# Kernel tuning notes

Hardware: AMD Instinct MI355X
Metric: run time of the kernel (lower is better)

## Reference

```python
import jax, jax.numpy as jnp
import numpy as np

EPS = 1e-5
QMAX = 127.0   # 8-bit symmetric: representable range [-128, 127]
QMIN = -128.0


def ste_round(x):
    # straight-through rounding (identity gradient)
    return x + jax.lax.stop_gradient(jnp.round(x) - x)


def setup_inputs() -> dict:
    key = jax.random.key(0)
    ks = jax.random.split(key, 7)
    N, C_in, C_out, H, W = 64, 256, 128, 56, 56
    x = jax.random.normal(ks[0], (N, C_in, H, W), jnp.float32)
    act_scaling_factor = jax.random.uniform(ks[1], (1,), jnp.float32, 0.02, 0.08)
    bn_weight = 1.0 + 0.3 * jax.random.normal(ks[2], (C_in,), jnp.float32)
    bn_bias = 0.1 * jax.random.normal(ks[3], (C_in,), jnp.float32)
    bn_mean = 0.1 * jax.random.normal(ks[4], (C_in,), jnp.float32)
    bn_var = jax.random.uniform(ks[5], (C_in,), jnp.float32, 0.5, 1.5)
    conv_weight = 0.05 * jax.random.normal(ks[6], (C_out, C_in, 1, 1), jnp.float32)
    return {
        "x": x,
        "act_scaling_factor": act_scaling_factor,
        "bn_weight": bn_weight,
        "bn_bias": bn_bias,
        "bn_mean": bn_mean,
        "bn_var": bn_var,
        "conv_weight": conv_weight,
    }


def _fwd(x, act_scaling_factor, bn_weight, bn_bias, bn_mean, bn_var, conv_weight):
    act_sf = act_scaling_factor.reshape(())

    # ---- QuantBn: fold BN, quantize folded scale per-channel (8-bit symmetric) ----
    inv_std = jax.lax.rsqrt(bn_var + EPS)
    scale = bn_weight * inv_std                    # [C_in]
    shift = bn_bias - bn_mean * scale              # [C_in]
    bn_sf = jnp.max(jnp.abs(scale)) / QMAX         # per-tensor bn weight scale
    scale_q = jnp.clip(ste_round(scale / bn_sf), QMIN, QMAX) * bn_sf
    bias_sf = bn_sf * act_sf                        # bias quantized at combined scale
    shift_q = ste_round(shift / bias_sf) * bias_sf
    x = x * scale_q[None, :, None, None] + shift_q[None, :, None, None]

    # ---- ReLU ----
    x = jnp.maximum(x, 0.0)

    # ---- QuantAct 1: per-tensor symmetric 8-bit requant ----
    sf1 = jnp.max(jnp.abs(x)) / QMAX
    x = jnp.clip(ste_round(x / sf1), QMIN, QMAX) * sf1

    # ---- QuantConv2d: per-output-channel 8-bit symmetric weight quant, 1x1 conv ----
    w_sf = jnp.max(jnp.abs(conv_weight), axis=(1, 2, 3)) / QMAX   # [C_out]
    w_q = jnp.clip(ste_round(conv_weight / w_sf[:, None, None, None]), QMIN, QMAX) \
          * w_sf[:, None, None, None]
    y = jax.lax.conv_general_dilated(
        x, w_q, window_strides=(1, 1), padding='VALID',
        dimension_numbers=('NCHW', 'OIHW', 'NCHW'))

    # ---- QuantAct 2 ----
    sf2 = jnp.max(jnp.abs(y)) / QMAX
    y = jnp.clip(ste_round(y / sf2), QMIN, QMAX) * sf2

    # ---- QuantAveragePool2d (2x2, stride 2): average in integer domain, re-round ----
    N, C, H, W = y.shape
    y_int = (y / sf2).reshape(N, C, H // 2, 2, W // 2, 2).mean(axis=(3, 5))
    out = ste_round(y_int) * sf2
    return out, sf2


def reference(x, act_scaling_factor, bn_weight, bn_bias, bn_mean, bn_var, conv_weight):
    return _fwd(x, act_scaling_factor, bn_weight, bn_bias, bn_mean, bn_var, conv_weight)
```

## Files before the change

### kernel.cpp

```cpp
#include <hip/hip_runtime.h>

#define QMAXF 127.0f
typedef int i32x4 __attribute__((ext_vector_type(4)));

__device__ __forceinline__ unsigned fkey(float f) {
  const unsigned b = __float_as_uint(f);
  return (b & 0x80000000u) ? ~b : (b | 0x80000000u);
}
__device__ __forceinline__ float fdec(unsigned u) {
  return __uint_as_float((u & 0x80000000u) ? (u & 0x7FFFFFFFu) : ~u);
}

__global__ __launch_bounds__(256, 8) void k1_minmax(
    const float* __restrict__ x, const float* __restrict__ actsf,
    const float* __restrict__ bnw, const float* __restrict__ bnb,
    const float* __restrict__ bnm, const float* __restrict__ bnv,
    const float* __restrict__ cw, unsigned* __restrict__ chanKmx,
    unsigned* __restrict__ chanKmn, float* __restrict__ scq,
    float* __restrict__ shq, float* __restrict__ wsf,
    signed char* __restrict__ wq8) {
  const int t = threadIdx.x, b = blockIdx.x;
  if (b == 2048) {
    __shared__ float red[4];
    float scale, shift;
    {
#pragma clang fp contract(off)
      float inv = 1.0f / sqrtf(bnv[t] + 1e-5f);
      scale = bnw[t] * inv;
      float tmp = bnm[t] * scale;
      shift = bnb[t] - tmp;
    }
    float a = fabsf(scale);
    for (int o = 32; o > 0; o >>= 1) a = fmaxf(a, __shfl_xor(a, o));
    if ((t & 63) == 0) red[t >> 6] = a;
    __syncthreads();
    const float amax = fmaxf(fmaxf(red[0], red[1]), fmaxf(red[2], red[3]));
    const float bn_sf = amax / QMAXF;
    scq[t] = fminf(fmaxf(rintf(scale / bn_sf), -128.f), 127.f) * bn_sf;
    const float bias_sf = bn_sf * actsf[0];
    shq[t] = rintf(shift / bias_sf) * bias_sf;
    const int r = t >> 1, half = t & 1;
    const float4* wrow = (const float4*)(cw + r * 256 + half * 128);
    float mx = 0.f;
#pragma unroll
    for (int j = 0; j < 32; ++j) {
      const float4 v = wrow[j];
      mx = fmaxf(mx, fmaxf(fmaxf(fabsf(v.x), fabsf(v.y)), fmaxf(fabsf(v.z), fabsf(v.w))));
    }
    mx = fmaxf(mx, __shfl_xor(mx, 1));
    const float wsf_v = mx / QMAXF;
    if (half == 0) wsf[r] = wsf_v;
    int* w8w = (int*)wq8;
#pragma unroll
    for (int j = 0; j < 32; ++j) {
      const float4 v = wrow[j];
      const float q0 = fminf(fmaxf(rintf(v.x / wsf_v), -128.f), 127.f);
      const float q1 = fminf(fmaxf(rintf(v.y / wsf_v), -128.f), 127.f);
      const float q2 = fminf(fmaxf(rintf(v.z / wsf_v), -128.f), 127.f);
      const float q3 = fminf(fmaxf(rintf(v.w / wsf_v), -128.f), 127.f);
      w8w[r * 64 + half * 32 + j] =
          ((int)q0 & 255) | (((int)q1 & 255) << 8) | (((int)q2 & 255) << 16) | (((int)q3 & 255) << 24);
    }
    return;
  }
  __shared__ float redmn[4][8], redmx[4][8];
  const int n = b >> 5, cg = b & 31;
  const float4* __restrict__ x4 = (const float4*)x + (long)(n * 256 + cg * 8) * 784;
  float mn[8], mx[8];
#pragma unroll
  for (int r = 0; r < 8; ++r) { mn[r] = __builtin_inff(); mx[r] = -__builtin_inff(); }
#pragma unroll
  for (int r = 0; r < 8; ++r) {
    const float4* row = x4 + r * 784;
    for (int j = t; j < 784; j += 256) {
      const float4 v = row[j];
      mn[r] = fminf(mn[r], fminf(fminf(v.x, v.y), fminf(v.z, v.w)));
      mx[r] = fmaxf(mx[r], fmaxf(fmaxf(v.x, v.y), fmaxf(v.z, v.w)));
    }
  }
#pragma unroll
  for (int r = 0; r < 8; ++r)
    for (int o = 32; o > 0; o >>= 1) {
      mn[r] = fminf(mn[r], __shfl_xor(mn[r], o));
      mx[r] = fmaxf(mx[r], __shfl_xor(mx[r], o));
    }
  if ((t & 63) == 0) {
#pragma unroll
    for (int r = 0; r < 8; ++r) { redmn[t >> 6][r] = mn[r]; redmx[t >> 6][r] = mx[r]; }
  }
  __syncthreads();
  if (t < 8) {
    const float fmn = fminf(fminf(redmn[0][t], redmn[1][t]), fminf(redmn[2][t], redmn[3][t]));
    const float fmx = fmaxf(fmaxf(redmx[0][t], redmx[1][t]), fmaxf(redmx[2][t], redmx[3][t]));
    atomicMax(&chanKmx[cg * 8 + t], fkey(fmx));
    atomicMax(&chanKmn[cg * 8 + t], ~fkey(fmn));
  }
}

__global__ __launch_bounds__(256, 4) void k2f_quant_gemm(
    const float* __restrict__ x, const float* __restrict__ scq,
    const float* __restrict__ shq, const unsigned* __restrict__ chanKmx,
    const unsigned* __restrict__ chanKmn, const signed char* __restrict__ wq8,
    const float* __restrict__ wsf, signed char* __restrict__ xqT,
    unsigned* __restrict__ gmax2K) {
  __shared__ int sw[64 * 64];
  __shared__ float comax[128];
  __shared__ float red[4];
  __shared__ float sf1s;
  const int t = threadIdx.x, w = t >> 6, l = t & 63, m = l & 15, g = l >> 4;
  const int blk = blockIdx.x, n = blk / 49, tt = blk - n * 49;

  {
    const float s = scq[t], sh = shq[t];
    const float xe = (s >= 0.f) ? fdec(chanKmx[t]) : fdec(~chanKmn[t]);
    float z;
    {
#pragma clang fp contract(off)
      z = xe * s + sh;
    }
    float mm = fmaxf(z, 0.f);
    for (int o = 32; o > 0; o >>= 1) mm = fmaxf(mm, __shfl_xor(mm, o));
    if (l == 0) red[w] = mm;
    __syncthreads();
    if (t == 0) sf1s = fmaxf(fmaxf(red[0], red[1]), fmaxf(red[2], red[3])) / QMAXF;
    __syncthreads();
  }
  const float sf1 = sf1s;
  const float* __restrict__ xb = x + (long)n * 802816 + tt * 64;

  signed char* __restrict__ dst = xqT + ((long)(n * 3136 + tt * 64)) * 256;
  {
    const int slot = t & 15, hwq = t >> 4;
    const int hw0 = hwq * 4, ci0 = slot * 16;
    int wbuf[4][4] = {{0, 0, 0, 0}, {0, 0, 0, 0}, {0, 0, 0, 0}, {0, 0, 0, 0}};
#pragma unroll
    for (int j = 0; j < 16; ++j) {
      const float4 v = *(const float4*)(xb + (long)(ci0 + j) * 3136 + hw0);
      const float s = scq[ci0 + j], sh = shq[ci0 + j];
      float z0, z1, z2, z3;
      {
#pragma clang fp contract(off)
        z0 = v.x * s + sh; z1 = v.y * s + sh; z2 = v.z * s + sh; z3 = v.w * s + sh;
      }
      const float q0 = fminf(fmaxf(rintf(fmaxf(z0, 0.f) / sf1), -128.f), 127.f);
      const float q1 = fminf(fmaxf(rintf(fmaxf(z1, 0.f) / sf1), -128.f), 127.f);
      const float q2 = fminf(fmaxf(rintf(fmaxf(z2, 0.f) / sf1), -128.f), 127.f);
      const float q3 = fminf(fmaxf(rintf(fmaxf(z3, 0.f) / sf1), -128.f), 127.f);
      wbuf[0][j >> 2] |= ((int)q0 & 255) << ((j & 3) * 8);
      wbuf[1][j >> 2] |= ((int)q1 & 255) << ((j & 3) * 8);
      wbuf[2][j >> 2] |= ((int)q2 & 255) << ((j & 3) * 8);
      wbuf[3][j >> 2] |= ((int)q3 & 255) << ((j & 3) * 8);
    }
#pragma unroll
    for (int dh = 0; dh < 4; ++dh) {
      const int hw = hw0 + dh;
      *(i32x4*)&sw[hw * 64 + ((slot ^ (hw & 7)) << 2)] = *(const i32x4*)wbuf[dh];
      *(i32x4*)(dst + hw * 256 + slot * 16) = *(const i32x4*)wbuf[dh];
    }
  }
  __syncthreads();

  i32x4 acc[2][4];
#pragma unroll
  for (int ct = 0; ct < 2; ++ct)
#pragma unroll
    for (int ht = 0; ht < 4; ++ht) acc[ct][ht] = (i32x4){0, 0, 0, 0};
#pragma unroll
  for (int ks = 0; ks < 4; ++ks) {
    const i32x4 wf0 = *(const i32x4*)(wq8 + (w * 32 + m) * 256 + ks * 64 + g * 16);
    const i32x4 wf1 = *(const i32x4*)(wq8 + (w * 32 + 16 + m) * 256 + ks * 64 + g * 16);
#pragma unroll
    for (int ht = 0; ht < 4; ++ht) {
      const int row = ht * 16 + m;
      const i32x4 xf = *(const i32x4*)&sw[row * 64 + (((ks * 4 + g) ^ (row & 7)) << 2)];
      acc[0][ht] = __builtin_amdgcn_mfma_i32_16x16x64_i8(wf0, xf, acc[0][ht], 0, 0, 0);
      acc[1][ht] = __builtin_amdgcn_mfma_i32_16x16x64_i8(wf1, xf, acc[1][ht], 0, 0, 0);
    }
  }

  int im[2][4];
#pragma unroll
  for (int ct = 0; ct < 2; ++ct)
#pragma unroll
    for (int r = 0; r < 4; ++r) {
      int v = 0;
#pragma unroll
      for (int ht = 0; ht < 4; ++ht) {
        int a = acc[ct][ht][r];
        a = a < 0 ? -a : a;
        v = a > v ? a : v;
      }
      im[ct][r] = v;
    }
#pragma unroll
  for (int o = 1; o < 16; o <<= 1)
#pragma unroll
    for (int ct = 0; ct < 2; ++ct)
#pragma unroll
      for (int r = 0; r < 4; ++r) {
        const int other = __shfl_xor(im[ct][r], o);
        im[ct][r] = other > im[ct][r] ? other : im[ct][r];
      }
  if (m == 0) {
#pragma unroll
    for (int ct = 0; ct < 2; ++ct)
#pragma unroll
      for (int r = 0; r < 4; ++r)
        comax[w * 32 + ct * 16 + g * 4 + r] = (float)im[ct][r];
  }
  __syncthreads();
  float v = 0.f;
  if (t < 128) v = comax[t] * (sf1 * wsf[t]);
  for (int o = 32; o > 0; o >>= 1) v = fmaxf(v, __shfl_xor(v, o));
  if (l == 0) red[w] = v;
  __syncthreads();
  if (t == 0)
    atomicMax(gmax2K, __float_as_uint(fmaxf(fmaxf(red[0], red[1]), fmaxf(red[2], red[3]))));
}

__global__ __launch_bounds__(256, 3) void k3_final(
    const signed char* __restrict__ xqT, const signed char* __restrict__ wq8,
    const float* __restrict__ wsf, const float* __restrict__ scq,
    const float* __restrict__ shq, const unsigned* __restrict__ chanKmx,
    const unsigned* __restrict__ chanKmn, const unsigned* __restrict__ gmax2K,
    float* __restrict__ out, float* __restrict__ outsf2) {
  __shared__ _Float16 q2[128 * 116];
  __shared__ float red[4];
  __shared__ float sf1s;
  const int t = threadIdx.x, w = t >> 6, l = t & 63;
  const int m = l & 15, g = l >> 4;
  const int blk = blockIdx.x;
  const int n = blk / 28, tt = blk - n * 28;

  {
    const float s = scq[t], sh = shq[t];
    const float xe = (s >= 0.f) ? fdec(chanKmx[t]) : fdec(~chanKmn[t]);
    float z;
    {
#pragma clang fp contract(off)
      z = xe * s + sh;
    }
    float mm = fmaxf(z, 0.f);
    for (int o = 32; o > 0; o >>= 1) mm = fmaxf(mm, __shfl_xor(mm, o));
    if (l == 0) red[w] = mm;
    __syncthreads();
    if (t == 0) sf1s = fmaxf(fmaxf(red[0], red[1]), fmaxf(red[2], red[3])) / QMAXF;
    __syncthreads();
  }
  const float sf1 = sf1s;
  const float sf2 = __uint_as_float(*gmax2K) / QMAXF;
  if (blk == 0 && t == 0) outsf2[0] = sf2;

  const signed char* __restrict__ xb = xqT + ((long)(n * 3136 + tt * 112)) * 256;
  i32x4 acc[2][7];
#pragma unroll
  for (int ct = 0; ct < 2; ++ct)
#pragma unroll
    for (int ht = 0; ht < 7; ++ht) acc[ct][ht] = (i32x4){0, 0, 0, 0};
#pragma unroll
  for (int ks = 0; ks < 4; ++ks) {
    const i32x4 wf0 = *(const i32x4*)(wq8 + (w * 32 + m) * 256 + ks * 64 + g * 16);
    const i32x4 wf1 = *(const i32x4*)(wq8 + (w * 32 + 16 + m) * 256 + ks * 64 + g * 16);
#pragma unroll
    for (int ht = 0; ht < 7; ++ht) {
      const i32x4 xf = *(const i32x4*)(xb + (ht * 16 + m) * 256 + ks * 64 + g * 16);
      acc[0][ht] = __builtin_amdgcn_mfma_i32_16x16x64_i8(wf0, xf, acc[0][ht], 0, 0, 0);
      acc[1][ht] = __builtin_amdgcn_mfma_i32_16x16x64_i8(wf1, xf, acc[1][ht], 0, 0, 0);
    }
  }
  float fac[2][4];
#pragma unroll
  for (int ct = 0; ct < 2; ++ct)
#pragma unroll
    for (int r = 0; r < 4; ++r)
      fac[ct][r] = sf1 * wsf[w * 32 + ct * 16 + g * 4 + r];
#pragma unroll
  for (int ct = 0; ct < 2; ++ct)
#pragma unroll
    for (int ht = 0; ht < 7; ++ht)
#pragma unroll
      for (int r = 0; r < 4; ++r) {
        const float y = (float)acc[ct][ht][r] * fac[ct][r];
        const float q = fminf(fmaxf(rintf(y / sf2), -128.f), 127.f);
        q2[(w * 32 + ct * 16 + g * 4 + r) * 116 + ht * 16 + m] = (_Float16)q;
      }
  __syncthreads();
  const long obase = (long)n * 100352 + tt * 28;
  for (int i = t; i < 3584; i += 256) {
    const unsigned co = (unsigned)i / 28u;
    const unsigned wo = (unsigned)i - co * 28u;
    const _Float16* row = q2 + co * 116;
    const float a = (float)row[2 * wo] + (float)row[2 * wo + 1] +
                    (float)row[56 + 2 * wo] + (float)row[56 + 2 * wo + 1];
    out[obase + (long)co * 784 + wo] = rintf(a * 0.25f) * sf2;
  }
}

extern "C" void kernel_launch(void* const* d_in, const int* in_sizes, int n_in,
                              void* d_out, int out_size, void* d_ws, size_t ws_size,
                              hipStream_t stream) {
  const float* x     = (const float*)d_in[0];
  const float* actsf = (const float*)d_in[1];
  const float* bnw   = (const float*)d_in[2];
  const float* bnb   = (const float*)d_in[3];
  const float* bnm   = (const float*)d_in[4];
  const float* bnv   = (const float*)d_in[5];
  const float* cw    = (const float*)d_in[6];
  float* out = (float*)d_out;
  char* ws = (char*)d_ws;

  unsigned* gmax2K    = (unsigned*)ws;
  unsigned* chanKmx   = (unsigned*)(ws + 256);
  unsigned* chanKmn   = (unsigned*)(ws + 1280);
  float* scq          = (float*)(ws + 4096);
  float* shq          = (float*)(ws + 5120);
  float* wsf          = (float*)(ws + 6144);
  signed char* wq8    = (signed char*)(ws + 8192);
  signed char* xqT    = (signed char*)(ws + 65536);
  float* outsf2       = out + (out_size - 1);

  hipMemsetAsync(ws, 0, 4096, stream);
  hipLaunchKernelGGL(k1_minmax, dim3(2049), dim3(256), 0, stream,
                     x, actsf, bnw, bnb, bnm, bnv, cw, chanKmx, chanKmn, scq, shq, wsf, wq8);
  hipLaunchKernelGGL(k2f_quant_gemm, dim3(3136), dim3(256), 0, stream,
                     x, scq, shq, chanKmx, chanKmn, wq8, wsf, xqT, gmax2K);
  hipLaunchKernelGGL(k3_final, dim3(1792), dim3(256), 0, stream,
                     xqT, wq8, wsf, scq, shq, chanKmx, chanKmn, gmax2K, out, outsf2);
}
```

Baseline: 160.1 us.

## Fuse quant-GEMM and final pass into persistent kernel with grid barrier

Merges the second and third kernels into one persistent kernel of 896 blocks that grid-strides over 1792 tiles of 112 pixels each. A software grid barrier (atomic counter plus generation flag) separates the phase that computes the global max from the pass that requantizes and pools. This removes one kernel launch and the tail between the two kernels, and enlarges the phase-1 tile from 64 to 112 pixels. The barrier assumes all 896 blocks are co-resident, so the kernel can deadlock if occupancy falls short. The persistent schedule also leaves the idle tail in each phase unaddressed.

```diff
diff --git a/kernel.cpp b/kernel.cpp
--- a/kernel.cpp
+++ b/kernel.cpp
@@ -1,6 +1,7 @@
 #include <hip/hip_runtime.h>
 
 #define QMAXF 127.0f
+#define NBLK 896u
 typedef int i32x4 __attribute__((ext_vector_type(4)));
 
 __device__ __forceinline__ unsigned fkey(float f) {
@@ -9,6 +10,22 @@
 }
 __device__ __forceinline__ float fdec(unsigned u) {
   return __uint_as_float((u & 0x80000000u) ? (u & 0x7FFFFFFFu) : ~u);
+}
+
+__device__ __forceinline__ void soft_sync(unsigned* cnt, unsigned* gen) {
+  __syncthreads();
+  if (threadIdx.x == 0) {
+    const unsigned g = __hip_atomic_load(gen, __ATOMIC_RELAXED, __HIP_MEMORY_SCOPE_AGENT);
+    const unsigned a = __hip_atomic_fetch_add(cnt, 1u, __ATOMIC_ACQ_REL, __HIP_MEMORY_SCOPE_AGENT);
+    if (a == NBLK - 1u) {
+      __hip_atomic_store(cnt, 0u, __ATOMIC_RELAXED, __HIP_MEMORY_SCOPE_AGENT);
+      __hip_atomic_fetch_add(gen, 1u, __ATOMIC_RELEASE, __HIP_MEMORY_SCOPE_AGENT);
+    } else {
+      while (__hip_atomic_load(gen, __ATOMIC_ACQUIRE, __HIP_MEMORY_SCOPE_AGENT) == g)
+        __builtin_amdgcn_s_sleep(2);
+    }
+  }
+  __syncthreads();
 }
 
 __global__ __launch_bounds__(256, 8) void k1_minmax(
@@ -97,18 +114,25 @@
   }
 }
 
-__global__ __launch_bounds__(256, 4) void k2f_quant_gemm(
+union K23Lds {
+  int sw[112 * 64];
+  _Float16 q2[128 * 116];
+};
+
+__global__ __launch_bounds__(256, 4) void k23(
     const float* __restrict__ x, const float* __restrict__ scq,
     const float* __restrict__ shq, const unsigned* __restrict__ chanKmx,
     const unsigned* __restrict__ chanKmn, const signed char* __restrict__ wq8,
     const float* __restrict__ wsf, signed char* __restrict__ xqT,
-    unsigned* __restrict__ gmax2K) {
-  __shared__ int sw[64 * 64];
+    unsigned* __restrict__ cnt, unsigned* __restrict__ gen,
+    unsigned* __restrict__ gmax2K, float* __restrict__ out,
+    float* __restrict__ outsf2) {
+  __shared__ K23Lds lds;
   __shared__ float comax[128];
   __shared__ float red[4];
   __shared__ float sf1s;
-  const int t = threadIdx.x, w = t >> 6, l = t & 63, m = l & 15, g = l >> 4;
-  const int blk = blockIdx.x, n = blk / 49, tt = blk - n * 49;
+  const int t = threadIdx.x, b = blockIdx.x;
+  const int w = t >> 6, l = t & 63, m = l & 15, g = l >> 4;
 
   {
     const float s = scq[t], sh = shq[t];
@@ -126,173 +150,152 @@
     __syncthreads();
   }
   const float sf1 = sf1s;
-  const float* __restrict__ xb = x + (long)n * 802816 + tt * 64;
-
-  signed char* __restrict__ dst = xqT + ((long)(n * 3136 + tt * 64)) * 256;
-  {
-    const int slot = t & 15, hwq = t >> 4;
-    const int hw0 = hwq * 4, ci0 = slot * 16;
-    int wbuf[4][4] = {{0, 0, 0, 0}, {0, 0, 0, 0}, {0, 0, 0, 0}, {0, 0, 0, 0}};
-#pragma unroll
-    for (int j = 0; j < 16; ++j) {
-      const float4 v = *(const float4*)(xb + (long)(ci0 + j) * 3136 + hw0);
-      const float s = scq[ci0 + j], sh = shq[ci0 + j];
-      float z0, z1, z2, z3;
-      {
+
+  for (int vb = b; vb < 1792; vb += (int)NBLK) {
+    const int n = vb / 28, tt = vb - n * 28;
+    const float* __restrict__ xb = x + (long)n * 802816 + tt * 112;
+    signed char* __restrict__ dst = xqT + ((long)(n * 3136 + tt * 112)) * 256;
+    for (int it = 0; it < 2; ++it) {
+      const int task = it * 256 + t;
+      if (task < 448) {
+        const int slot = task & 15, hwq = task >> 4;
+        const int hw0 = hwq * 4, ci0 = slot * 16;
+        int wbuf[4][4] = {{0, 0, 0, 0}, {0, 0, 0, 0}, {0, 0, 0, 0}, {0, 0, 0, 0}};
+#pragma unroll
+        for (int j = 0; j < 16; ++j) {
+          const float4 v = *(const float4*)(xb + (long)(ci0 + j) * 3136 + hw0);
+          const float s = scq[ci0 + j], sh = shq[ci0 + j];
+          float z0, z1, z2, z3;
+          {
 #pragma clang fp contract(off)
-        z0 = v.x * s + sh; z1 = v.y * s + sh; z2 = v.z * s + sh; z3 = v.w * s + sh;
+            z0 = v.x * s + sh; z1 = v.y * s + sh; z2 = v.z * s + sh; z3 = v.w * s + sh;
+          }
+          const float q0 = fminf(fmaxf(rintf(fmaxf(z0, 0.f) / sf1), -128.f), 127.f);
+          const float q1 = fminf(fmaxf(rintf(fmaxf(z1, 0.f) / sf1), -128.f), 127.f);
+          const float q2 = fminf(fmaxf(rintf(fmaxf(z2, 0.f) / sf1), -128.f), 127.f);
+          const float q3 = fminf(fmaxf(rintf(fmaxf(z3, 0.f) / sf1), -128.f), 127.f);
+          wbuf[0][j >> 2] |= ((int)q0 & 255) << ((j & 3) * 8);
+          wbuf[1][j >> 2] |= ((int)q1 & 255) << ((j & 3) * 8);
+          wbuf[2][j >> 2] |= ((int)q2 & 255) << ((j & 3) * 8);
+          wbuf[3][j >> 2] |= ((int)q3 & 255) << ((j & 3) * 8);
+        }
+#pragma unroll
+        for (int dh = 0; dh < 4; ++dh) {
+          const int hw = hw0 + dh;
+          *(i32x4*)&lds.sw[hw * 64 + ((slot ^ (hw & 7)) << 2)] = *(const i32x4*)wbuf[dh];
+          *(i32x4*)(dst + hw * 256 + slot * 16) = *(const i32x4*)wbuf[dh];
+        }
       }
-      const float q0 = fminf(fmaxf(rintf(fmaxf(z0, 0.f) / sf1), -128.f), 127.f);
-      const float q1 = fminf(fmaxf(rintf(fmaxf(z1, 0.f) / sf1), -128.f), 127.f);
-      const float q2 = fminf(fmaxf(rintf(fmaxf(z2, 0.f) / sf1), -128.f), 127.f);
-      const float q3 = fminf(fmaxf(rintf(fmaxf(z3, 0.f) / sf1), -128.f), 127.f);
-      wbuf[0][j >> 2] |= ((int)q0 & 255) << ((j & 3) * 8);
-      wbuf[1][j >> 2] |= ((int)q1 & 255) << ((j & 3) * 8);
-      wbuf[2][j >> 2] |= ((int)q2 & 255) << ((j & 3) * 8);
-      wbuf[3][j >> 2] |= ((int)q3 & 255) << ((j & 3) * 8);
-    }
-#pragma unroll
-    for (int dh = 0; dh < 4; ++dh) {
-      const int hw = hw0 + dh;
-      *(i32x4*)&sw[hw * 64 + ((slot ^ (hw & 7)) << 2)] = *(const i32x4*)wbuf[dh];
-      *(i32x4*)(dst + hw * 256 + slot * 16) = *(const i32x4*)wbuf[dh];
-    }
-  }
-  __syncthreads();
-
-  i32x4 acc[2][4];
-#pragma unroll
-  for (int ct = 0; ct < 2; ++ct)
-#pragma unroll
-    for (int ht = 0; ht < 4; ++ht) acc[ct][ht] = (i32x4){0, 0, 0, 0};
-#pragma unroll
-  for (int ks = 0; ks < 4; ++ks) {
-    const i32x4 wf0 = *(const i32x4*)(wq8 + (w * 32 + m) * 256 + ks * 64 + g * 16);
-    const i32x4 wf1 = *(const i32x4*)(wq8 + (w * 32 + 16 + m) * 256 + ks * 64 + g * 16);
-#pragma unroll
-    for (int ht = 0; ht < 4; ++ht) {
-      const int row = ht * 16 + m;
-      const i32x4 xf = *(const i32x4*)&sw[row * 64 + (((ks * 4 + g) ^ (row & 7)) << 2)];
-      acc[0][ht] = __builtin_amdgcn_mfma_i32_16x16x64_i8(wf0, xf, acc[0][ht], 0, 0, 0);
-      acc[1][ht] = __builtin_amdgcn_mfma_i32_16x16x64_i8(wf1, xf, acc[1][ht], 0, 0, 0);
-    }
-  }
-
-  int im[2][4];
-#pragma unroll
-  for (int ct = 0; ct < 2; ++ct)
-#pragma unroll
-    for (int r = 0; r < 4; ++r) {
-      int v = 0;
-#pragma unroll
-      for (int ht = 0; ht < 4; ++ht) {
-        int a = acc[ct][ht][r];
-        a = a < 0 ? -a : a;
-        v = a > v ? a : v;
+    }
+    __syncthreads();
+    i32x4 acc[2][7];
+#pragma unroll
+    for (int ct = 0; ct < 2; ++ct)
+#pragma unroll
+      for (int ht = 0; ht < 7; ++ht) acc[ct][ht] = (i32x4){0, 0, 0, 0};
+#pragma unroll
+    for (int ks = 0; ks < 4; ++ks) {
+      const i32x4 wf0 = *(const i32x4*)(wq8 + (w * 32 + m) * 256 + ks * 64 + g * 16);
+      const i32x4 wf1 = *(const i32x4*)(wq8 + (w * 32 + 16 + m) * 256 + ks * 64 + g * 16);
+#pragma unroll
+      for (int ht = 0; ht < 7; ++ht) {
+        const int row = ht * 16 + m;
+        const i32x4 xf = *(const i32x4*)&lds.sw[row * 64 + (((ks * 4 + g) ^ (row & 7)) << 2)];
+        acc[0][ht] = __builtin_amdgcn_mfma_i32_16x16x64_i8(wf0, xf, acc[0][ht], 0, 0, 0);
+        acc[1][ht] = __builtin_amdgcn_mfma_i32_16x16x64_i8(wf1, xf, acc[1][ht], 0, 0, 0);
       }
-      im[ct][r] = v;
-    }
-#pragma unroll
-  for (int o = 1; o < 16; o <<= 1)
+    }
+    int im[2][4];
 #pragma unroll
     for (int ct = 0; ct < 2; ++ct)
 #pragma unroll
       for (int r = 0; r < 4; ++r) {
-        const int other = __shfl_xor(im[ct][r], o);
-        im[ct][r] = other > im[ct][r] ? other : im[ct][r];
+        int v = 0;
+#pragma unroll
+        for (int ht = 0; ht < 7; ++ht) {
+          int a = acc[ct][ht][r];
+          a = a < 0 ? -a : a;
+          v = a > v ? a : v;
+        }
+        im[ct][r] = v;
       }
-  if (m == 0) {
+#pragma unroll
+    for (int o = 1; o < 16; o <<= 1)
+#pragma unroll
+      for (int ct = 0; ct < 2; ++ct)
+#pragma unroll
+        for (int r = 0; r < 4; ++r) {
+          const int other = __shfl_xor(im[ct][r], o);
+          im[ct][r] = other > im[ct][r] ? other : im[ct][r];
+        }
+    if (m == 0) {
+#pragma unroll
+      for (int ct = 0; ct < 2; ++ct)
+#pragma unroll
+        for (int r = 0; r < 4; ++r)
+          comax[w * 32 + ct * 16 + g * 4 + r] = (float)im[ct][r];
+    }
+    __syncthreads();
+    float v = 0.f;
+    if (t < 128) v = comax[t] * (sf1 * wsf[t]);
+    for (int o = 32; o > 0; o >>= 1) v = fmaxf(v, __shfl_xor(v, o));
+    if (l == 0) red[w] = v;
+    __syncthreads();
+    if (t == 0)
+      atomicMax(gmax2K, __float_as_uint(fmaxf(fmaxf(red[0], red[1]), fmaxf(red[2], red[3]))));
+    __syncthreads();
+  }
+  soft_sync(cnt, gen);
+
+  const float sf2 =
+      __uint_as_float(__hip_atomic_load(gmax2K, __ATOMIC_RELAXED, __HIP_MEMORY_SCOPE_AGENT)) / QMAXF;
+  if (b == 0 && t == 0) outsf2[0] = sf2;
+  for (int vb = b; vb < 1792; vb += (int)NBLK) {
+    const int n = vb / 28, tt = vb - n * 28;
+    const signed char* __restrict__ xb = xqT + ((long)(n * 3136 + tt * 112)) * 256;
+    i32x4 acc[2][7];
+#pragma unroll
+    for (int ct = 0; ct < 2; ++ct)
+#pragma unroll
+      for (int ht = 0; ht < 7; ++ht) acc[ct][ht] = (i32x4){0, 0, 0, 0};
+#pragma unroll
+    for (int ks = 0; ks < 4; ++ks) {
+      const i32x4 wf0 = *(const i32x4*)(wq8 + (w * 32 + m) * 256 + ks * 64 + g * 16);
+      const i32x4 wf1 = *(const i32x4*)(wq8 + (w * 32 + 16 + m) * 256 + ks * 64 + g * 16);
+#pragma unroll
+      for (int ht = 0; ht < 7; ++ht) {
+        const i32x4 xf = *(const i32x4*)(xb + (ht * 16 + m) * 256 + ks * 64 + g * 16);
+        acc[0][ht] = __builtin_amdgcn_mfma_i32_16x16x64_i8(wf0, xf, acc[0][ht], 0, 0, 0);
+        acc[1][ht] = __builtin_amdgcn_mfma_i32_16x16x64_i8(wf1, xf, acc[1][ht], 0, 0, 0);
+      }
+    }
+    float fac[2][4];
 #pragma unroll
     for (int ct = 0; ct < 2; ++ct)
 #pragma unroll
       for (int r = 0; r < 4; ++r)
-        comax[w * 32 + ct * 16 + g * 4 + r] = (float)im[ct][r];
-  }
-  __syncthreads();
-  float v = 0.f;
-  if (t < 128) v = comax[t] * (sf1 * wsf[t]);
-  for (int o = 32; o > 0; o >>= 1) v = fmaxf(v, __shfl_xor(v, o));
-  if (l == 0) red[w] = v;
-  __syncthreads();
-  if (t == 0)
-    atomicMax(gmax2K, __float_as_uint(fmaxf(fmaxf(red[0], red[1]), fmaxf(red[2], red[3]))));
-}
-
-__global__ __launch_bounds__(256, 3) void k3_final(
-    const signed char* __restrict__ xqT, const signed char* __restrict__ wq8,
-    const float* __restrict__ wsf, const float* __restrict__ scq,
-    const float* __restrict__ shq, const unsigned* __restrict__ chanKmx,
-    const unsigned* __restrict__ chanKmn, const unsigned* __restrict__ gmax2K,
-    float* __restrict__ out, float* __restrict__ outsf2) {
-  __shared__ _Float16 q2[128 * 116];
-  __shared__ float red[4];
-  __shared__ float sf1s;
-  const int t = threadIdx.x, w = t >> 6, l = t & 63;
-  const int m = l & 15, g = l >> 4;
-  const int blk = blockIdx.x;
-  const int n = blk / 28, tt = blk - n * 28;
-
-  {
-    const float s = scq[t], sh = shq[t];
-    const float xe = (s >= 0.f) ? fdec(chanKmx[t]) : fdec(~chanKmn[t]);
-    float z;
-    {
-#pragma clang fp contract(off)
-      z = xe * s + sh;
-    }
-    float mm = fmaxf(z, 0.f);
-    for (int o = 32; o > 0; o >>= 1) mm = fmaxf(mm, __shfl_xor(mm, o));
-    if (l == 0) red[w] = mm;
-    __syncthreads();
-    if (t == 0) sf1s = fmaxf(fmaxf(red[0], red[1]), fmaxf(red[2], red[3])) / QMAXF;
-    __syncthreads();
-  }
-  const float sf1 = sf1s;
-  const float sf2 = __uint_as_float(*gmax2K) / QMAXF;
-  if (blk == 0 && t == 0) outsf2[0] = sf2;
-
-  const signed char* __restrict__ xb = xqT + ((long)(n * 3136 + tt * 112)) * 256;
-  i32x4 acc[2][7];
-#pragma unroll
-  for (int ct = 0; ct < 2; ++ct)
-#pragma unroll
-    for (int ht = 0; ht < 7; ++ht) acc[ct][ht] = (i32x4){0, 0, 0, 0};
-#pragma unroll
-  for (int ks = 0; ks < 4; ++ks) {
-    const i32x4 wf0 = *(const i32x4*)(wq8 + (w * 32 + m) * 256 + ks * 64 + g * 16);
-    const i32x4 wf1 = *(const i32x4*)(wq8 + (w * 32 + 16 + m) * 256 + ks * 64 + g * 16);
-#pragma unroll
-    for (int ht = 0; ht < 7; ++ht) {
-      const i32x4 xf = *(const i32x4*)(xb + (ht * 16 + m) * 256 + ks * 64 + g * 16);
-      acc[0][ht] = __builtin_amdgcn_mfma_i32_16x16x64_i8(wf0, xf, acc[0][ht], 0, 0, 0);
-      acc[1][ht] = __builtin_amdgcn_mfma_i32_16x16x64_i8(wf1, xf, acc[1][ht], 0, 0, 0);
-    }
-  }
-  float fac[2][4];
-#pragma unroll
-  for (int ct = 0; ct < 2; ++ct)
-#pragma unroll
-    for (int r = 0; r < 4; ++r)
-      fac[ct][r] = sf1 * wsf[w * 32 + ct * 16 + g * 4 + r];
-#pragma unroll
-  for (int ct = 0; ct < 2; ++ct)
-#pragma unroll
-    for (int ht = 0; ht < 7; ++ht)
-#pragma unroll
-      for (int r = 0; r < 4; ++r) {
-        const float y = (float)acc[ct][ht][r] * fac[ct][r];
-        const float q = fminf(fmaxf(rintf(y / sf2), -128.f), 127.f);
-        q2[(w * 32 + ct * 16 + g * 4 + r) * 116 + ht * 16 + m] = (_Float16)q;
-      }
-  __syncthreads();
-  const long obase = (long)n * 100352 + tt * 28;
-  for (int i = t; i < 3584; i += 256) {
-    const unsigned co = (unsigned)i / 28u;
-    const unsigned wo = (unsigned)i - co * 28u;
-    const _Float16* row = q2 + co * 116;
-    const float a = (float)row[2 * wo] + (float)row[2 * wo + 1] +
-                    (float)row[56 + 2 * wo] + (float)row[56 + 2 * wo + 1];
-    out[obase + (long)co * 784 + wo] = rintf(a * 0.25f) * sf2;
+        fac[ct][r] = sf1 * wsf[w * 32 + ct * 16 + g * 4 + r];
+#pragma unroll
+    for (int ct = 0; ct < 2; ++ct)
+#pragma unroll
+      for (int ht = 0; ht < 7; ++ht)
+#pragma unroll
+        for (int r = 0; r < 4; ++r) {
+          const float y = (float)acc[ct][ht][r] * fac[ct][r];
+          const float q = fminf(fmaxf(rintf(y / sf2), -128.f), 127.f);
+          lds.q2[(w * 32 + ct * 16 + g * 4 + r) * 116 + ht * 16 + m] = (_Float16)q;
+        }
+    __syncthreads();
+    const long obase = (long)n * 100352 + tt * 28;
+    for (int i = t; i < 3584; i += 256) {
+      const unsigned co = (unsigned)i / 28u;
+      const unsigned wo = (unsigned)i - co * 28u;
+      const _Float16* row = lds.q2 + co * 116;
+      const float a = (float)row[2 * wo] + (float)row[2 * wo + 1] +
+                      (float)row[56 + 2 * wo] + (float)row[56 + 2 * wo + 1];
+      out[obase + (long)co * 784 + wo] = rintf(a * 0.25f) * sf2;
+    }
+    __syncthreads();
   }
 }
 
@@ -309,7 +312,9 @@
   float* out = (float*)d_out;
   char* ws = (char*)d_ws;
 
-  unsigned* gmax2K    = (unsigned*)ws;
+  unsigned* cnt       = (unsigned*)ws;
+  unsigned* gen       = (unsigned*)(ws + 4);
+  unsigned* gmax2K    = (unsigned*)(ws + 8);
   unsigned* chanKmx   = (unsigned*)(ws + 256);
   unsigned* chanKmn   = (unsigned*)(ws + 1280);
   float* scq          = (float*)(ws + 4096);
@@ -322,8 +327,7 @@
   hipMemsetAsync(ws, 0, 4096, stream);
   hipLaunchKernelGGL(k1_minmax, dim3(2049), dim3(256), 0, stream,
                      x, actsf, bnw, bnb, bnm, bnv, cw, chanKmx, chanKmn, scq, shq, wsf, wq8);
-  hipLaunchKernelGGL(k2f_quant_gemm, dim3(3136), dim3(256), 0, stream,
-                     x, scq, shq, chanKmx, chanKmn, wq8, wsf, xqT, gmax2K);
-  hipLaunchKernelGGL(k3_final, dim3(1792), dim3(256), 0, stream,
-                     xqT, wq8, wsf, scq, shq, chanKmx, chanKmn, gmax2K, out, outsf2);
-}
+  hipLaunchKernelGGL(k23, dim3(NBLK), dim3(256), 0, stream,
+                     x, scq, shq, chanKmx, chanKmn, wq8, wsf, xqT,
+                     cnt, gen, gmax2K, out, outsf2);
+}
```

After: 456.1 us. +184.9%, slower.
